# Optimization experiments

Hardware: AMD Instinct MI355X
Metric: run time of the kernel (lower is better)

Reference implementation:

```python
import jax, jax.numpy as jnp
import numpy as np

N_USERS = 100000
N_ITEMS = 50000
N_ENT = 80000            # items + tags (tags = 30000)
N_NODES = N_USERS + N_ENT
N_EDGES = 800000
D = 64
N_LAYERS = 2


def _center_net(embs, idx, n, W1, b1, W2, b2):
    # CenterIntersection: linear+relu, linear, segment softmax, weighted segment sum
    act = jnp.maximum(embs @ W1.T + b1, 0.0)
    logits = act @ W2.T + b2
    m = jax.ops.segment_max(logits, idx, num_segments=n)
    e = jnp.exp(logits - m[idx])
    s = jax.ops.segment_sum(e, idx, num_segments=n)
    att = e / s[idx]
    return jax.ops.segment_sum(att * embs, idx, num_segments=n)


def _offset_net(embs, idx, mask, n, use_min, W1, b1, W2, b2):
    # BoxOffsetIntersection restricted to edges where mask is True
    mf = mask[:, None].astype(embs.dtype)
    act = jnp.maximum(embs @ W1.T + b1, 0.0) * mf
    cnt = jax.ops.segment_sum(mask.astype(embs.dtype), idx, num_segments=n)
    mean = jax.ops.segment_sum(act, idx, num_segments=n) / jnp.maximum(cnt, 1.0)[:, None]
    gate = jax.nn.sigmoid(mean @ W2.T + b2)
    if use_min:
        src = jnp.where(mask[:, None], embs, jnp.inf)
        red = jax.ops.segment_min(src, idx, num_segments=n)
    else:
        src = jnp.where(mask[:, None], embs, -jnp.inf)
        red = jax.ops.segment_max(src, idx, num_segments=n)
    red = jnp.where(jnp.isfinite(red), red, 0.0)  # torch_scatter fills empty segments with 0
    return red * gate


def setup_inputs() -> dict:
    key = jax.random.key(0)
    ks = jax.random.split(key, 10)
    s = 0.05  # xavier-like scale
    return {
        "user_emb": jax.random.normal(ks[0], (N_USERS, D), jnp.float32),
        "user_offset_emb": jax.random.normal(ks[1], (N_USERS, D), jnp.float32),
        "item_emb": jax.random.normal(ks[2], (N_ENT, D), jnp.float32),
        "item_offset_emb": jax.random.normal(ks[3], (N_ENT, D), jnp.float32),
        "cW1": jax.random.normal(ks[4], (D, D), jnp.float32) * s,
        "cb1": jnp.zeros((D,), jnp.float32),
        "cW2": jax.random.normal(ks[5], (D, D), jnp.float32) * s,
        "cb2": jnp.zeros((D,), jnp.float32),
        "oW1": jax.random.normal(ks[6], (D, D), jnp.float32) * s,
        "ob1": jnp.zeros((D,), jnp.float32),
        "oW2": jax.random.normal(ks[7], (D, D), jnp.float32) * s,
        "ob2": jnp.zeros((D,), jnp.float32),
        "head": jax.random.randint(ks[8], (N_EDGES,), 0, N_NODES, jnp.int32),
        "tail": jax.random.randint(ks[9], (N_EDGES,), 0, N_NODES, jnp.int32),
    }


def reference(user_emb, user_offset_emb, item_emb, item_offset_emb,
              cW1, cb1, cW2, cb2, oW1, ob1, oW2, ob2, head, tail):
    all_embs = jnp.concatenate([user_emb, item_emb], axis=0)              # [N_NODES, D]
    all_off = jnp.maximum(jnp.concatenate([user_offset_emb, item_offset_emb], axis=0), 0.0)
    uu_idx = jnp.concatenate([jnp.arange(N_USERS), jnp.arange(N_USERS)])
    uu_mask = jnp.ones((2 * N_USERS,), bool)
    m_inter = (tail >= N_USERS) & (head < N_USERS) & (tail < N_USERS + N_ITEMS)
    m_ut = (head < N_USERS) & (tail >= N_USERS + N_ITEMS)
    m_item = (head >= N_USERS) & (head < N_USERS + N_ITEMS)
    m_tag = head >= N_USERS + N_ITEMS
    for _ in range(N_LAYERS):
        h_embs = all_embs[tail]                                           # [E, D] gather
        agg_emb = _center_net(h_embs, head, N_NODES, cW1, cb1, cW2, cb2)
        edge_off = jnp.maximum(all_off[tail], 0.0)                        # [E, D]
        inter_u = _offset_net(edge_off, head, m_inter, N_NODES, True, oW1, ob1, oW2, ob2)[:N_USERS]
        ut_u = _offset_net(edge_off, head, m_ut, N_NODES, False, oW1, ob1, oW2, ob2)[:N_USERS]
        item_o = _offset_net(edge_off, head, m_item, N_NODES, False, oW1, ob1, oW2, ob2)[N_USERS:N_USERS + N_ITEMS]
        tag_o = _offset_net(edge_off, head, m_tag, N_NODES, True, oW1, ob1, oW2, ob2)[N_USERS + N_ITEMS:]
        uo_cat = jnp.concatenate([inter_u, ut_u], axis=0)                 # [2*N_USERS, D]
        user_o = jnp.maximum(_offset_net(uo_cat, uu_idx, uu_mask, N_USERS, False, oW1, ob1, oW2, ob2), 0.0)
        agg_off = jnp.concatenate([user_o, item_o, tag_o], axis=0)
        agg_emb = agg_emb / jnp.maximum(jnp.linalg.norm(agg_emb, axis=1, keepdims=True), 1e-12)  # F.normalize
        all_embs = agg_emb
        all_off = agg_off
    return (all_embs[:N_USERS], all_off[:N_USERS], all_embs[N_USERS:], all_off[N_USERS:])
```

## Files before the change

### kernel.cpp

```cpp
#include <hip/hip_runtime.h>
#include <hip/hip_fp16.h>
#include <math.h>

#define NU 100000
#define NI 50000
#define NENT 80000
#define NN 180000
#define NEDGE 800000
#define SCAN_NB ((NN + 1023) / 1024)
#define UFIN_BLKS ((NU + 63) / 64)
#define EFIN_BLKS (NENT / 64)
#define NODE_BLKS ((NN / 16 + 3) / 4)
#define HIST_BLKS ((NEDGE + 255) / 256)

typedef _Float16 f16x4 __attribute__((ext_vector_type(4)));
typedef _Float16 f16x2 __attribute__((ext_vector_type(2)));
typedef float f32x4 __attribute__((ext_vector_type(4)));

__device__ __forceinline__ float sigmoid_f(float x) { return 1.0f / (1.0f + __expf(-x)); }
__device__ __forceinline__ unsigned pack2(float a, float b) {
    __half2 h = __floats2half2_rn(a, b);
    return *(unsigned*)&h;
}
__device__ __forceinline__ f16x2 u2h2(unsigned u) { union { unsigned u; f16x2 h; } x; x.u = u; return x.h; }
__device__ __forceinline__ float fdot2f(f16x2 a, f16x2 b, float c) {
#if __has_builtin(__builtin_amdgcn_fdot2)
    return __builtin_amdgcn_fdot2(a, b, c, false);
#else
    return (float)a[0] * (float)b[0] + (float)a[1] * (float)b[1] + c;
#endif
}
__device__ __forceinline__ _Float16 hminf(_Float16 a, _Float16 b) { return a < b ? a : b; }
__device__ __forceinline__ _Float16 hmaxf(_Float16 a, _Float16 b) { return a > b ? a : b; }

template<typename T>
__device__ __forceinline__ f16x4 ldfrag(const T* __restrict__ p) {
    if constexpr (sizeof(T) == 2) {
        return *(const f16x4*)p;
    } else {
        float4 v = *(const float4*)p;
        f16x4 r; r[0] = (_Float16)v.x; r[1] = (_Float16)v.y; r[2] = (_Float16)v.z; r[3] = (_Float16)v.w;
        return r;
    }
}
template<typename T>
__device__ __forceinline__ f16x4 ldfragr(const T* __restrict__ p) {
    if constexpr (sizeof(T) == 2) {
        f16x4 v = *(const f16x4*)p;
        #pragma unroll
        for (int i = 0; i < 4; ++i) v[i] = hmaxf(v[i], (_Float16)0.f);
        return v;
    } else {
        float4 v = *(const float4*)p;
        f16x4 r;
        r[0] = (_Float16)fmaxf(v.x, 0.f); r[1] = (_Float16)fmaxf(v.y, 0.f);
        r[2] = (_Float16)fmaxf(v.z, 0.f); r[3] = (_Float16)fmaxf(v.w, 0.f);
        return r;
    }
}
__device__ __forceinline__ f16x4 fragp(const _Float16* __restrict__ Wp, int dt, int ks, int lane) {
    return *(const f16x4*)(Wp + (((dt * 4 + ks) * 64 + lane) << 2));
}
__device__ __forceinline__ f32x4 mmw(f16x4 wfrag, f16x4 xfrag, f32x4 c) {
    return __builtin_amdgcn_mfma_f32_16x16x16f16(wfrag, xfrag, c, 0, 0, 0);
}
__device__ __forceinline__ f32x4 bias4(const float* __restrict__ b, int dt, int lk) {
    float4 v = *(const float4*)(b + dt * 16 + lk * 4);
    f32x4 r = {v.x, v.y, v.z, v.w};
    return r;
}

__global__ __launch_bounds__(256) void prep_w(
    const float* __restrict__ W0, const float* __restrict__ W1,
    const float* __restrict__ W2, const float* __restrict__ W3,
    _Float16* __restrict__ out)
{
    int idx = blockIdx.x * 256 + threadIdx.x;
    int mat = idx >> 12, wi = idx & 4095;
    const float* W = (mat == 0) ? W0 : (mat == 1) ? W1 : (mat == 2) ? W2 : W3;
    int tile = wi >> 8;
    int dt = tile >> 2, ks = tile & 3;
    int ln = (wi >> 2) & 63, j = wi & 3;
    int lr = ln & 15, lk = ln >> 4;
    out[idx] = (_Float16)W[(size_t)(dt * 16 + lr) * 64 + ks * 16 + lk * 4 + j];
}

template<typename T, bool HIST>
__global__ __launch_bounds__(256) void node_pass(
    const T* __restrict__ embU, const T* __restrict__ embE,
    const T* __restrict__ offU, const T* __restrict__ offE,
    const _Float16* __restrict__ cW1f, const float* __restrict__ cb1,
    const _Float16* __restrict__ cW2f, const float* __restrict__ cb2,
    const _Float16* __restrict__ oW1f, const float* __restrict__ ob1,
    unsigned* __restrict__ packedA, unsigned* __restrict__ packedB,
    const int* __restrict__ head, int* __restrict__ counts)
{
    if (HIST && blockIdx.x >= NODE_BLKS) {
        int e = ((int)blockIdx.x - NODE_BLKS) * 256 + threadIdx.x;
        if (e < NEDGE) atomicAdd(&counts[head[e]], 1);
        return;
    }
    int lane = threadIdx.x & 63, wid = threadIdx.x >> 6;
    int n0 = (blockIdx.x * 4 + wid) * 16;
    if (n0 >= NN) return;
    int lr = lane & 15, lk = lane >> 4;
    const T* eb; const T* ob;
    if (n0 < NU) { eb = embU + (size_t)n0 * 64; ob = offU + (size_t)n0 * 64; }
    else         { eb = embE + (size_t)(n0 - NU) * 64; ob = offE + (size_t)(n0 - NU) * 64; }

    f16x4 ax[4], axo[4];
    #pragma unroll
    for (int ks = 0; ks < 4; ++ks) {
        ax[ks]  = ldfrag(eb + (size_t)lr * 64 + ks * 16 + lk * 4);
        axo[ks] = ldfragr(ob + (size_t)lr * 64 + ks * 16 + lk * 4);
    }
    f32x4 a1c[4];
    #pragma unroll
    for (int dt = 0; dt < 4; ++dt) {
        f32x4 c = bias4(cb1, dt, lk);
        #pragma unroll
        for (int ks = 0; ks < 4; ++ks) c = mmw(fragp(cW1f, dt, ks, lane), ax[ks], c);
        a1c[dt] = c;
    }
    f16x4 a1f[4];
    #pragma unroll
    for (int ks = 0; ks < 4; ++ks)
        #pragma unroll
        for (int r = 0; r < 4; ++r) a1f[ks][r] = (_Float16)fmaxf(a1c[ks][r], 0.f);
    f32x4 lg[4];
    #pragma unroll
    for (int dt = 0; dt < 4; ++dt) {
        f32x4 c = bias4(cb2, dt, lk);
        #pragma unroll
        for (int ks = 0; ks < 4; ++ks) c = mmw(fragp(cW2f, dt, ks, lane), a1f[ks], c);
        lg[dt] = c;
    }
    f32x4 ao[4];
    #pragma unroll
    for (int dt = 0; dt < 4; ++dt) {
        f32x4 c = bias4(ob1, dt, lk);
        #pragma unroll
        for (int ks = 0; ks < 4; ++ks) c = mmw(fragp(oW1f, dt, ks, lane), axo[ks], c);
        ao[dt] = c;
    }
    #pragma unroll
    for (int dt = 0; dt < 4; ++dt) {
        uint4 ua, ub;
        unsigned* pa = &ua.x; unsigned* pb = &ub.x;
        #pragma unroll
        for (int r = 0; r < 4; ++r) {
            float ev = __expf(lg[dt][r]);
            pa[r] = pack2(ev, ev * (float)ax[dt][r]);
            pb[r] = pack2(fmaxf(ao[dt][r], 0.f), (float)axo[dt][r]);
        }
        size_t idx = (size_t)(n0 + lr) * 64 + dt * 16 + lk * 4;
        *(uint4*)(packedA + idx) = ua;
        *(uint4*)(packedB + idx) = ub;
    }
}

__global__ __launch_bounds__(1024) void scan_local(const int* __restrict__ counts,
                                                   int* __restrict__ excl, int* __restrict__ partials) {
    __shared__ int wsum[16];
    int tid = threadIdx.x, lane = tid & 63, wid = tid >> 6;
    int i = blockIdx.x * 1024 + tid;
    int v = (i < NN) ? counts[i] : 0;
    int s = v;
    #pragma unroll
    for (int d = 1; d < 64; d <<= 1) { int u = __shfl_up(s, d, 64); if (lane >= d) s += u; }
    if (lane == 63) wsum[wid] = s;
    __syncthreads();
    if (wid == 0 && lane < 16) {
        int w = wsum[lane];
        #pragma unroll
        for (int d = 1; d < 16; d <<= 1) { int u = __shfl_up(w, d, 64); if (lane >= d) w += u; }
        wsum[lane] = w;
    }
    __syncthreads();
    int base = wid ? wsum[wid - 1] : 0;
    if (i < NN) excl[i] = base + s - v;
    if (tid == 1023) partials[blockIdx.x] = wsum[15];
}

__global__ __launch_bounds__(256) void scan_carry(const int* __restrict__ partials, int* __restrict__ carries) {
    __shared__ int ws[4];
    int tid = threadIdx.x, lane = tid & 63, wid = tid >> 6;
    int v = (tid < SCAN_NB) ? partials[tid] : 0;
    int s = v;
    #pragma unroll
    for (int d = 1; d < 64; d <<= 1) { int u = __shfl_up(s, d, 64); if (lane >= d) s += u; }
    if (lane == 63) ws[wid] = s;
    __syncthreads();
    int add = 0;
    for (int w = 0; w < wid; ++w) add += ws[w];
    if (tid < SCAN_NB) carries[tid] = add + s - v;
}

__global__ __launch_bounds__(1024) void scan_add(int* __restrict__ excl, const int* __restrict__ carries,
                                                 int* __restrict__ cursor) {
    int i = blockIdx.x * 1024 + threadIdx.x;
    if (i < NN) { int o = excl[i] + carries[blockIdx.x]; excl[i] = o; cursor[i] = o; }
    if (i == 0) excl[NN] = NEDGE;
}

__global__ __launch_bounds__(256) void scatter_k(const int* __restrict__ head, const int* __restrict__ tail,
                                                 int* __restrict__ cursor, int* __restrict__ sorted_t) {
    int e = blockIdx.x * 256 + threadIdx.x;
    if (e < NEDGE) { int pos = atomicAdd(&cursor[head[e]], 1); sorted_t[pos] = tail[e]; }
}

template<bool OUT16>
__global__ __launch_bounds__(256) void seg_pass(
    const unsigned* __restrict__ packedA, const unsigned* __restrict__ packedB,
    const int* __restrict__ offsets, const int* __restrict__ sorted_t,
    void* __restrict__ embOutU_, void* __restrict__ embOutE_,
    _Float16* __restrict__ meanI, _Float16* __restrict__ redI,
    _Float16* __restrict__ meanU, _Float16* __restrict__ redU,
    _Float16* __restrict__ meanE, _Float16* __restrict__ redE)
{
    int lane = threadIdx.x & 63;
    int h = blockIdx.x * 4 + (threadIdx.x >> 6);
    int beg = offsets[h], end = offsets[h + 1];
    bool isUser = (h < NU);
    bool entMin = (h >= NU + NI);
    const f16x2 SEL_LO = {(_Float16)1.0f, (_Float16)0.0f};
    const f16x2 SEL_HI = {(_Float16)0.0f, (_Float16)1.0f};
    float num = 0.f, den = 0.f, s_i = 0.f, s_u = 0.f;
    const _Float16 HINF = u2h2(0x7C007C00u)[0];
    _Float16 m_i = (isUser || entMin) ? HINF : (_Float16)0.f;
    _Float16 m_u = (_Float16)0.f;
    int c_i = 0, c_u = 0;

    const char* pA = (const char*)packedA;
    const char* pB = (const char*)packedB;
    int loff = lane << 2;

#define LOADQ(t, a, b)                                                          \
    do {                                                                        \
        a = *(const unsigned*)(pA + ((size_t)(unsigned)(t) << 8) + loff);       \
        if (!isUser || (t) >= NU)                                               \
            b = *(const unsigned*)(pB + ((size_t)(unsigned)(t) << 8) + loff);   \
    } while (0)

#define CONSUME(tc, qa, qb)                                                     \
    do {                                                                        \
        f16x2 ea = u2h2(qa);                                                    \
        den = fdot2f(ea, SEL_LO, den);                                          \
        num = fdot2f(ea, SEL_HI, num);                                          \
        if (isUser) {                                                           \
            if ((tc) >= NU) {                                                   \
                f16x2 ab = u2h2(qb);                                            \
                if ((tc) < NU + NI) { s_i = fdot2f(ab, SEL_LO, s_i); m_i = hminf(m_i, ab[1]); c_i++; } \
                else                { s_u = fdot2f(ab, SEL_LO, s_u); m_u = hmaxf(m_u, ab[1]); c_u++; } \
            }                                                                   \
        } else {                                                                \
            f16x2 ab = u2h2(qb);                                                \
            s_i = fdot2f(ab, SEL_LO, s_i); c_i++;                               \
            m_i = entMin ? hminf(m_i, ab[1]) : hmaxf(m_i, ab[1]);               \
        }                                                                       \
    } while (0)

    for (int base = beg; base < end; base += 64) {
        int rem = end - base; if (rem > 64) rem = 64;
        int tv = sorted_t[base + (lane < rem ? lane : 0)];
        int tA = 0, tB = 0; unsigned aA = 0, aB = 0, bA = 0, bB = 0;
        tA = __builtin_amdgcn_readlane(tv, 0);
        LOADQ(tA, aA, bA);
        if (rem > 1) { tB = __builtin_amdgcn_readlane(tv, 1); LOADQ(tB, aB, bB); }
        int j = 0;
        for (; j + 2 <= rem; j += 2) {
            CONSUME(tA, aA, bA);
            if (j + 2 < rem) { tA = __builtin_amdgcn_readlane(tv, j + 2); LOADQ(tA, aA, bA); }
            CONSUME(tB, aB, bB);
            if (j + 3 < rem) { tB = __builtin_amdgcn_readlane(tv, j + 3); LOADQ(tB, aB, bB); }
        }
        if (j < rem) CONSUME(tA, aA, bA);
    }
#undef LOADQ
#undef CONSUME

    float v = (den > 0.f) ? num / den : 0.f;
    float sq = v * v;
    #pragma unroll
    for (int m = 32; m; m >>= 1) sq += __shfl_xor(sq, m, 64);
    v = v / fmaxf(sqrtf(sq), 1e-12f);

    float m_if = (float)m_i;
    if (m_if > 1e37f) m_if = 0.f;
    float rc_i = __builtin_amdgcn_rcpf(fmaxf((float)c_i, 1.f));
    if (isUser) {
        size_t r = (size_t)h * 64 + lane;
        if constexpr (OUT16) ((_Float16*)embOutU_)[r] = (_Float16)v;
        else                 ((float*)embOutU_)[r] = v;
        float rc_u = __builtin_amdgcn_rcpf(fmaxf((float)c_u, 1.f));
        meanI[r] = (_Float16)(s_i * rc_i);
        redI[r]  = (_Float16)m_if;
        meanU[r] = (_Float16)(s_u * rc_u);
        redU[r]  = m_u;
    } else {
        size_t r = (size_t)(h - NU) * 64 + lane;
        if constexpr (OUT16) ((_Float16*)embOutE_)[r] = (_Float16)v;
        else                 ((float*)embOutE_)[r] = v;
        meanE[r] = (_Float16)(s_i * rc_i);
        redE[r]  = (_Float16)m_if;
    }
}

template<bool OUT16>
__global__ __launch_bounds__(256) void fin_pass(
    const _Float16* __restrict__ meanI, const _Float16* __restrict__ redI,
    const _Float16* __restrict__ meanU, const _Float16* __restrict__ redU,
    const _Float16* __restrict__ meanE, const _Float16* __restrict__ redE,
    const _Float16* __restrict__ oW1f, const float* __restrict__ ob1,
    const _Float16* __restrict__ oW2f, const float* __restrict__ ob2,
    void* __restrict__ outOffU_, void* __restrict__ entOff_)
{
    int lane = threadIdx.x & 63, wid = threadIdx.x >> 6;
    int lr = lane & 15, lk = lane >> 4;

    if (blockIdx.x >= UFIN_BLKS) {
        int n0 = (((int)blockIdx.x - UFIN_BLKS) * 4 + wid) * 16;
        if (n0 >= NENT) return;
        f16x4 am[4];
        #pragma unroll
        for (int ks = 0; ks < 4; ++ks) am[ks] = *(const f16x4*)(meanE + (size_t)(n0 + lr) * 64 + ks * 16 + lk * 4);
        #pragma unroll
        for (int dt = 0; dt < 4; ++dt) {
            f32x4 c = bias4(ob2, dt, lk);
            #pragma unroll
            for (int ks = 0; ks < 4; ++ks) c = mmw(fragp(oW2f, dt, ks, lane), am[ks], c);
            size_t idx = (size_t)(n0 + lr) * 64 + dt * 16 + lk * 4;
            f16x4 red = *(const f16x4*)(redE + idx);
            if constexpr (OUT16) {
                f16x4 o;
                #pragma unroll
                for (int r = 0; r < 4; ++r) o[r] = (_Float16)((float)red[r] * sigmoid_f(c[r]));
                *(f16x4*)((_Float16*)entOff_ + idx) = o;
            } else {
                float4 o;
                float* po = &o.x;
                #pragma unroll
                for (int r = 0; r < 4; ++r) po[r] = (float)red[r] * sigmoid_f(c[r]);
                *(float4*)((float*)entOff_ + idx) = o;
            }
        }
        return;
    }

    int u0 = (blockIdx.x * 4 + wid) * 16;
    if (u0 >= NU) return;

    f16x4 W1f[4][4], W2f[4][4];
    #pragma unroll
    for (int dt = 0; dt < 4; ++dt)
        #pragma unroll
        for (int ks = 0; ks < 4; ++ks) {
            W1f[dt][ks] = fragp(oW1f, dt, ks, lane);
            W2f[dt][ks] = fragp(oW2f, dt, ks, lane);
        }

    f16x4 am[4];
    f32x4 iu[4], uu[4];
    #pragma unroll
    for (int ks = 0; ks < 4; ++ks) am[ks] = *(const f16x4*)(meanI + (size_t)(u0 + lr) * 64 + ks * 16 + lk * 4);
    #pragma unroll
    for (int dt = 0; dt < 4; ++dt) {
        f32x4 c = bias4(ob2, dt, lk);
        #pragma unroll
        for (int ks = 0; ks < 4; ++ks) c = mmw(W2f[dt][ks], am[ks], c);
        f16x4 red = *(const f16x4*)(redI + (size_t)(u0 + lr) * 64 + dt * 16 + lk * 4);
        #pragma unroll
        for (int r = 0; r < 4; ++r) iu[dt][r] = (float)red[r] * sigmoid_f(c[r]);
    }
    #pragma unroll
    for (int ks = 0; ks < 4; ++ks) am[ks] = *(const f16x4*)(meanU + (size_t)(u0 + lr) * 64 + ks * 16 + lk * 4);
    #pragma unroll
    for (int dt = 0; dt < 4; ++dt) {
        f32x4 c = bias4(ob2, dt, lk);
        #pragma unroll
        for (int ks = 0; ks < 4; ++ks) c = mmw(W2f[dt][ks], am[ks], c);
        f16x4 red = *(const f16x4*)(redU + (size_t)(u0 + lr) * 64 + dt * 16 + lk * 4);
        #pragma unroll
        for (int r = 0; r < 4; ++r) uu[dt][r] = (float)red[r] * sigmoid_f(c[r]);
    }
    f16x4 iuf[4], uuf[4];
    #pragma unroll
    for (int ks = 0; ks < 4; ++ks)
        #pragma unroll
        for (int r = 0; r < 4; ++r) { iuf[ks][r] = (_Float16)iu[ks][r]; uuf[ks][r] = (_Float16)uu[ks][r]; }
    f32x4 mn[4];
    #pragma unroll
    for (int dt = 0; dt < 4; ++dt) {
        f32x4 c = bias4(ob1, dt, lk);
        #pragma unroll
        for (int ks = 0; ks < 4; ++ks) c = mmw(W1f[dt][ks], iuf[ks], c);
        #pragma unroll
        for (int r = 0; r < 4; ++r) mn[dt][r] = fmaxf(c[r], 0.f);
    }
    #pragma unroll
    for (int dt = 0; dt < 4; ++dt) {
        f32x4 c = bias4(ob1, dt, lk);
        #pragma unroll
        for (int ks = 0; ks < 4; ++ks) c = mmw(W1f[dt][ks], uuf[ks], c);
        #pragma unroll
        for (int r = 0; r < 4; ++r) mn[dt][r] = 0.5f * (mn[dt][r] + fmaxf(c[r], 0.f));
    }
    f16x4 mnf[4];
    #pragma unroll
    for (int ks = 0; ks < 4; ++ks)
        #pragma unroll
        for (int r = 0; r < 4; ++r) mnf[ks][r] = (_Float16)mn[ks][r];
    #pragma unroll
    for (int dt = 0; dt < 4; ++dt) {
        f32x4 c = bias4(ob2, dt, lk);
        #pragma unroll
        for (int ks = 0; ks < 4; ++ks) c = mmw(W2f[dt][ks], mnf[ks], c);
        size_t idx = (size_t)(u0 + lr) * 64 + dt * 16 + lk * 4;
        if constexpr (OUT16) {
            f16x4 o;
            #pragma unroll
            for (int r = 0; r < 4; ++r)
                o[r] = (_Float16)fmaxf(fmaxf(iu[dt][r], uu[dt][r]) * sigmoid_f(c[r]), 0.f);
            *(f16x4*)((_Float16*)outOffU_ + idx) = o;
        } else {
            float4 o;
            float* po = &o.x;
            #pragma unroll
            for (int r = 0; r < 4; ++r)
                po[r] = fmaxf(fmaxf(iu[dt][r], uu[dt][r]) * sigmoid_f(c[r]), 0.f);
            *(float4*)((float*)outOffU_ + idx) = o;
        }
    }
}

extern "C" void kernel_launch(void* const* d_in, const int* in_sizes, int n_in,
                              void* d_out, int out_size, void* d_ws, size_t ws_size,
                              hipStream_t stream)
{
    const float* user_emb = (const float*)d_in[0];
    const float* user_off = (const float*)d_in[1];
    const float* item_emb = (const float*)d_in[2];
    const float* item_off = (const float*)d_in[3];
    const float* cW1 = (const float*)d_in[4];
    const float* cb1 = (const float*)d_in[5];
    const float* cW2 = (const float*)d_in[6];
    const float* cb2 = (const float*)d_in[7];
    const float* oW1 = (const float*)d_in[8];
    const float* ob1 = (const float*)d_in[9];
    const float* oW2 = (const float*)d_in[10];
    const float* ob2 = (const float*)d_in[11];
    const int* head = (const int*)d_in[12];
    const int* tail = (const int*)d_in[13];
    float* out = (float*)d_out;

    const size_t SZ = (size_t)NN * 64;
    _Float16* A16   = (_Float16*)d_ws;
    _Float16* B16   = A16 + SZ;
    unsigned* packedA = (unsigned*)(B16 + SZ);
    unsigned* packedB = packedA + SZ;
    _Float16* meanI_h = (_Float16*)(packedB + SZ);
    _Float16* redI_h  = meanI_h + (size_t)NU * 64;
    _Float16* meanU_h = redI_h + (size_t)NU * 64;
    _Float16* redU_h  = meanU_h + (size_t)NU * 64;
    _Float16* meanE_h = redU_h + (size_t)NU * 64;
    _Float16* redE_h  = meanE_h + (size_t)NENT * 64;
    _Float16* wpre    = redE_h + (size_t)NENT * 64;
    int* counts   = (int*)(wpre + 4 * 4096);
    int* offsets  = counts + NN;
    int* cursor   = offsets + NN + 1;
    int* sorted_t = cursor + NN;
    int* partials = sorted_t + NEDGE;
    int* carries  = partials + SCAN_NB;

    const _Float16* cW1f = wpre;
    const _Float16* cW2f = wpre + 4096;
    const _Float16* oW1f = wpre + 8192;
    const _Float16* oW2f = wpre + 12288;

    prep_w<<<64, 256, 0, stream>>>(cW1, cW2, oW1, oW2, wpre);
    hipMemsetAsync(counts, 0, NN * sizeof(int), stream);

    node_pass<float, true><<<NODE_BLKS + HIST_BLKS, 256, 0, stream>>>(
        user_emb, item_emb, user_off, item_off,
        cW1f, cb1, cW2f, cb2, oW1f, ob1, packedA, packedB, head, counts);

    scan_local<<<SCAN_NB, 1024, 0, stream>>>(counts, offsets, partials);
    scan_carry<<<1, 256, 0, stream>>>(partials, carries);
    scan_add<<<SCAN_NB, 1024, 0, stream>>>(offsets, carries, cursor);
    scatter_k<<<(NEDGE + 255) / 256, 256, 0, stream>>>(head, tail, cursor, sorted_t);

    seg_pass<true><<<NN / 4, 256, 0, stream>>>(
        packedA, packedB, offsets, sorted_t,
        A16, A16 + (size_t)NU * 64,
        meanI_h, redI_h, meanU_h, redU_h, meanE_h, redE_h);
    fin_pass<true><<<UFIN_BLKS + EFIN_BLKS, 256, 0, stream>>>(
        meanI_h, redI_h, meanU_h, redU_h, meanE_h, redE_h,
        oW1f, ob1, oW2f, ob2, B16, B16 + (size_t)NU * 64);

    node_pass<_Float16, false><<<NODE_BLKS, 256, 0, stream>>>(
        A16, A16 + (size_t)NU * 64, B16, B16 + (size_t)NU * 64,
        cW1f, cb1, cW2f, cb2, oW1f, ob1, packedA, packedB, head, counts);
    seg_pass<false><<<NN / 4, 256, 0, stream>>>(
        packedA, packedB, offsets, sorted_t,
        out, out + (size_t)2 * NU * 64,
        meanI_h, redI_h, meanU_h, redU_h, meanE_h, redE_h);
    fin_pass<false><<<UFIN_BLKS + EFIN_BLKS, 256, 0, stream>>>(
        meanI_h, redI_h, meanU_h, redU_h, meanE_h, redE_h,
        oW1f, ob1, oW2f, ob2, out + (size_t)NU * 64, out + ((size_t)2 * NU + NENT) * 64);
}
```

Measured before the change: 408.9 us.

## Merge weight prep with counts zeroing, split histogram, pre-shift sorted tail indices

The memset of the counts array moves into the weight-prep kernel, removing one runtime call. The edge histogram is pulled out of node_pass into its own kernel, and node_pass now runs after CSR construction. scatter_k stores tail indices already shifted by 8 as byte offsets, so seg_pass skips the shift and compares against pre-scaled thresholds. The cost is an extra kernel launch, and the histogram no longer runs concurrently with the node matmuls.

```diff
diff --git a/kernel.cpp b/kernel.cpp
--- a/kernel.cpp
+++ b/kernel.cpp
@@ -11,7 +11,8 @@
 #define UFIN_BLKS ((NU + 63) / 64)
 #define EFIN_BLKS (NENT / 64)
 #define NODE_BLKS ((NN / 16 + 3) / 4)
-#define HIST_BLKS ((NEDGE + 255) / 256)
+#define NU8 (NU * 256)
+#define NUI8 ((NU + NI) * 256)
 
 typedef _Float16 f16x4 __attribute__((ext_vector_type(4)));
 typedef _Float16 f16x2 __attribute__((ext_vector_type(2)));
@@ -70,36 +71,34 @@
     return r;
 }
 
-__global__ __launch_bounds__(256) void prep_w(
+__global__ __launch_bounds__(256) void prep_zero(
     const float* __restrict__ W0, const float* __restrict__ W1,
     const float* __restrict__ W2, const float* __restrict__ W3,
-    _Float16* __restrict__ out)
+    _Float16* __restrict__ out, int* __restrict__ counts)
 {
     int idx = blockIdx.x * 256 + threadIdx.x;
-    int mat = idx >> 12, wi = idx & 4095;
-    const float* W = (mat == 0) ? W0 : (mat == 1) ? W1 : (mat == 2) ? W2 : W3;
-    int tile = wi >> 8;
-    int dt = tile >> 2, ks = tile & 3;
-    int ln = (wi >> 2) & 63, j = wi & 3;
-    int lr = ln & 15, lk = ln >> 4;
-    out[idx] = (_Float16)W[(size_t)(dt * 16 + lr) * 64 + ks * 16 + lk * 4 + j];
-}
-
-template<typename T, bool HIST>
+    if (idx < 16384) {
+        int mat = idx >> 12, wi = idx & 4095;
+        const float* W = (mat == 0) ? W0 : (mat == 1) ? W1 : (mat == 2) ? W2 : W3;
+        int tile = wi >> 8;
+        int dt = tile >> 2, ks = tile & 3;
+        int ln = (wi >> 2) & 63, j = wi & 3;
+        int lr = ln & 15, lk = ln >> 4;
+        out[idx] = (_Float16)W[(size_t)(dt * 16 + lr) * 64 + ks * 16 + lk * 4 + j];
+    }
+    int z = idx - 16384;
+    if (z >= 0 && z < NN) counts[z] = 0;
+}
+
+template<typename T>
 __global__ __launch_bounds__(256) void node_pass(
     const T* __restrict__ embU, const T* __restrict__ embE,
     const T* __restrict__ offU, const T* __restrict__ offE,
     const _Float16* __restrict__ cW1f, const float* __restrict__ cb1,
     const _Float16* __restrict__ cW2f, const float* __restrict__ cb2,
     const _Float16* __restrict__ oW1f, const float* __restrict__ ob1,
-    unsigned* __restrict__ packedA, unsigned* __restrict__ packedB,
-    const int* __restrict__ head, int* __restrict__ counts)
+    unsigned* __restrict__ packedA, unsigned* __restrict__ packedB)
 {
-    if (HIST && blockIdx.x >= NODE_BLKS) {
-        int e = ((int)blockIdx.x - NODE_BLKS) * 256 + threadIdx.x;
-        if (e < NEDGE) atomicAdd(&counts[head[e]], 1);
-        return;
-    }
     int lane = threadIdx.x & 63, wid = threadIdx.x >> 6;
     int n0 = (blockIdx.x * 4 + wid) * 16;
     if (n0 >= NN) return;
@@ -159,6 +158,11 @@
     }
 }
 
+__global__ __launch_bounds__(256) void hist_k(const int* __restrict__ head, int* __restrict__ counts) {
+    int e = blockIdx.x * 256 + threadIdx.x;
+    if (e < NEDGE) atomicAdd(&counts[head[e]], 1);
+}
+
 __global__ __launch_bounds__(1024) void scan_local(const int* __restrict__ counts,
                                                    int* __restrict__ excl, int* __restrict__ partials) {
     __shared__ int wsum[16];
@@ -206,7 +210,7 @@
 __global__ __launch_bounds__(256) void scatter_k(const int* __restrict__ head, const int* __restrict__ tail,
                                                  int* __restrict__ cursor, int* __restrict__ sorted_t) {
     int e = blockIdx.x * 256 + threadIdx.x;
-    if (e < NEDGE) { int pos = atomicAdd(&cursor[head[e]], 1); sorted_t[pos] = tail[e]; }
+    if (e < NEDGE) { int pos = atomicAdd(&cursor[head[e]], 1); sorted_t[pos] = tail[e] << 8; }
 }
 
 template<bool OUT16>
@@ -235,23 +239,23 @@
     const char* pB = (const char*)packedB;
     int loff = lane << 2;
 
-#define LOADQ(t, a, b)                                                          \
+#define LOADQ(toff, a, b)                                                       \
     do {                                                                        \
-        a = *(const unsigned*)(pA + ((size_t)(unsigned)(t) << 8) + loff);       \
-        if (!isUser || (t) >= NU)                                               \
-            b = *(const unsigned*)(pB + ((size_t)(unsigned)(t) << 8) + loff);   \
+        a = *(const unsigned*)(pA + (size_t)(unsigned)(toff) + loff);           \
+        if (!isUser || (toff) >= NU8)                                           \
+            b = *(const unsigned*)(pB + (size_t)(unsigned)(toff) + loff);       \
     } while (0)
 
-#define CONSUME(tc, qa, qb)                                                     \
+#define CONSUME(toff, qa, qb)                                                   \
     do {                                                                        \
         f16x2 ea = u2h2(qa);                                                    \
         den = fdot2f(ea, SEL_LO, den);                                          \
         num = fdot2f(ea, SEL_HI, num);                                          \
         if (isUser) {                                                           \
-            if ((tc) >= NU) {                                                   \
+            if ((toff) >= NU8) {                                                \
                 f16x2 ab = u2h2(qb);                                            \
-                if ((tc) < NU + NI) { s_i = fdot2f(ab, SEL_LO, s_i); m_i = hminf(m_i, ab[1]); c_i++; } \
-                else                { s_u = fdot2f(ab, SEL_LO, s_u); m_u = hmaxf(m_u, ab[1]); c_u++; } \
+                if ((toff) < NUI8) { s_i = fdot2f(ab, SEL_LO, s_i); m_i = hminf(m_i, ab[1]); c_i++; } \
+                else               { s_u = fdot2f(ab, SEL_LO, s_u); m_u = hmaxf(m_u, ab[1]); c_u++; } \
             }                                                                   \
         } else {                                                                \
             f16x2 ab = u2h2(qb);                                                \
@@ -477,18 +481,17 @@
     const _Float16* oW1f = wpre + 8192;
     const _Float16* oW2f = wpre + 12288;
 
-    prep_w<<<64, 256, 0, stream>>>(cW1, cW2, oW1, oW2, wpre);
-    hipMemsetAsync(counts, 0, NN * sizeof(int), stream);
-
-    node_pass<float, true><<<NODE_BLKS + HIST_BLKS, 256, 0, stream>>>(
-        user_emb, item_emb, user_off, item_off,
-        cW1f, cb1, cW2f, cb2, oW1f, ob1, packedA, packedB, head, counts);
-
+    prep_zero<<<64 + (NN + 255) / 256, 256, 0, stream>>>(cW1, cW2, oW1, oW2,
+                                                         (_Float16*)wpre, counts);
+    hist_k<<<(NEDGE + 255) / 256, 256, 0, stream>>>(head, counts);
     scan_local<<<SCAN_NB, 1024, 0, stream>>>(counts, offsets, partials);
     scan_carry<<<1, 256, 0, stream>>>(partials, carries);
     scan_add<<<SCAN_NB, 1024, 0, stream>>>(offsets, carries, cursor);
     scatter_k<<<(NEDGE + 255) / 256, 256, 0, stream>>>(head, tail, cursor, sorted_t);
 
+    node_pass<float><<<NODE_BLKS, 256, 0, stream>>>(
+        user_emb, item_emb, user_off, item_off,
+        cW1f, cb1, cW2f, cb2, oW1f, ob1, packedA, packedB);
     seg_pass<true><<<NN / 4, 256, 0, stream>>>(
         packedA, packedB, offsets, sorted_t,
         A16, A16 + (size_t)NU * 64,
@@ -497,9 +500,9 @@
         meanI_h, redI_h, meanU_h, redU_h, meanE_h, redE_h,
         oW1f, ob1, oW2f, ob2, B16, B16 + (size_t)NU * 64);
 
-    node_pass<_Float16, false><<<NODE_BLKS, 256, 0, stream>>>(
+    node_pass<_Float16><<<NODE_BLKS, 256, 0, stream>>>(
         A16, A16 + (size_t)NU * 64, B16, B16 + (size_t)NU * 64,
-        cW1f, cb1, cW2f, cb2, oW1f, ob1, packedA, packedB, head, counts);
+        cW1f, cb1, cW2f, cb2, oW1f, ob1, packedA, packedB);
     seg_pass<false><<<NN / 4, 256, 0, stream>>>(
         packedA, packedB, offsets, sorted_t,
         out, out + (size_t)2 * NU * 64,
```

Measured after the change: 415.3 us. Within noise of the previous version (+1.6%).
